# Kernel optimization log

Measured on AMD Instinct MI355X. Metric: run time of the kernel, lower is better.

Reference implementation:

```python
import jax, jax.numpy as jnp
import numpy as np

N = 100000   # vertices
T = 128      # temporal depth
E = 1600000  # edges (avg degree 16)
K = 9        # conv kernel size
PAD = 4      # 'same' padding -> T preserved
L = 3        # number of layers


def setup_inputs() -> dict:
    key = jax.random.key(0)
    ks = jax.random.split(key, 6)
    x = jax.random.normal(ks[0], (N, T), dtype=jnp.float32)
    edge_index = jax.random.randint(ks[1], (2, E), 0, N, dtype=jnp.int32)
    conv_w = jax.random.normal(ks[2], (L, 1, 1, K), dtype=jnp.float32) * (1.0 / np.sqrt(K))
    conv_b = jax.random.normal(ks[3], (L, 1), dtype=jnp.float32) * 0.1
    W_out = jax.random.normal(ks[4], (3, N), dtype=jnp.float32) * (1.0 / np.sqrt(N))
    b_out = jax.random.normal(ks[5], (3,), dtype=jnp.float32) * 0.1
    return {"x": x, "edge_index": edge_index, "conv_w": conv_w,
            "conv_b": conv_b, "W_out": W_out, "b_out": b_out}


def _conv1d(x, w, b):
    # x: [N, T], w: [1, 1, K] (OIH), b: [1]; torch Conv1d = cross-correlation.
    y = jax.lax.conv_general_dilated(
        x[:, None, :], w, window_strides=(1,), padding=[(PAD, PAD)],
        dimension_numbers=("NCH", "OIH", "NCH"))
    return y[:, 0, :] + b  # [N, T]


def reference(x, edge_index, conv_w, conv_b, W_out, b_out):
    # add_self_loops: append (i, i) for every node
    loop = jnp.arange(N, dtype=edge_index.dtype)
    src = jnp.concatenate([edge_index[0], loop])  # message sources
    dst = jnp.concatenate([edge_index[1], loop])  # aggregation targets
    # in-degree counts (>=1 due to self loops) for mean aggregation
    cnt = jax.ops.segment_sum(jnp.ones(src.shape, jnp.float32), dst,
                              num_segments=N)[:, None]  # [N, 1]
    for i in range(L):
        h = _conv1d(x, conv_w[i], conv_b[i])                    # [N, T]
        s = jax.ops.segment_sum(h[src], dst, num_segments=N)    # scatter-sum of gathered msgs
        x = jax.nn.relu(s / cnt)                                # mean aggr + relu
    x = x.reshape(-1, N)            # [T, N] (row-major view like torch .view)
    return x @ W_out.T + b_out      # [T, 3]
```

## Files before the change

### kernel.cpp

```cpp
#include <hip/hip_runtime.h>

#define NN 100000
#define TT 128
#define EE 1600000
#define KK 9
#define PADK 4
#define NSPLIT 16

#define BSH 7
#define BMASK 127
#define NBUCK 782
#define BCAP 2560
#define BINB 782
#define CVTB 12500

typedef _Float16 f16;
typedef __attribute__((ext_vector_type(2))) _Float16 f16x2;
typedef __attribute__((ext_vector_type(4))) _Float16 f16x4;
typedef __attribute__((ext_vector_type(8))) _Float16 f16x8;

union HU8 { f16x8 h; int4 i; };

__global__ void bin_cvt_kernel(const int* __restrict__ ei, int* __restrict__ gcursor,
                               unsigned int* __restrict__ binned,
                               const float4* __restrict__ x, f16x4* __restrict__ x16) {
    __shared__ int hist[NBUCK];
    __shared__ int gbase[NBUCK];
    int tid = threadIdx.x;

    if (blockIdx.x >= BINB) {
        int i = (blockIdx.x - BINB) * 256 + tid;
        float4 v = x[i];
        f16x4 o;
        o.x = (f16)v.x; o.y = (f16)v.y; o.z = (f16)v.z; o.w = (f16)v.w;
        x16[i] = o;
        return;
    }

    for (int i = tid; i < NBUCK; i += 256) hist[i] = 0;
    __syncthreads();
    int base = blockIdx.x * 2048;
    unsigned int val[8];
    int bkt[8];
    int rank[8];
#pragma unroll
    for (int k = 0; k < 8; k++) {
        int e = base + k * 256 + tid;
        bkt[k] = -1;
        if (e < EE) {
            int s = ei[e];
            int d = ei[EE + e];
            bkt[k] = d >> BSH;
            val[k] = ((unsigned int)(d & BMASK) << 20) | (unsigned int)s;
            rank[k] = atomicAdd(&hist[bkt[k]], 1);
        }
    }
    __syncthreads();
    for (int i = tid; i < NBUCK; i += 256)
        gbase[i] = hist[i] ? atomicAdd(&gcursor[i], hist[i]) : 0;
    __syncthreads();
#pragma unroll
    for (int k = 0; k < 8; k++) {
        if (bkt[k] >= 0)
            binned[(size_t)bkt[k] * BCAP + gbase[bkt[k]] + rank[k]] = val[k];
    }
}

__global__ void scanpart_kernel(const int* __restrict__ gcursor, int* __restrict__ part,
                                int* __restrict__ offsets) {
    __shared__ int sm[256];
    int tid = threadIdx.x;
    int base = tid * 4;
    int v[4];
    int s = 0;
#pragma unroll
    for (int k = 0; k < 4; k++) {
        int i = base + k;
        v[k] = (i < NBUCK) ? gcursor[i] : 0;
        s += v[k];
    }
    sm[tid] = s;
    __syncthreads();
    for (int off = 1; off < 256; off <<= 1) {
        int t = (tid >= off) ? sm[tid - off] : 0;
        __syncthreads();
        sm[tid] += t;
        __syncthreads();
    }
    int run = (tid == 0) ? 0 : sm[tid - 1];
#pragma unroll
    for (int k = 0; k < 4; k++) {
        int i = base + k;
        if (i < NBUCK) part[i] = run;
        run += v[k];
    }
    if (tid == 0) offsets[NN] = EE;
}

__global__ void bucket_csr_kernel(const unsigned int* __restrict__ binned,
                                  const int* __restrict__ gcursor,
                                  const int* __restrict__ part,
                                  int* __restrict__ offsets,
                                  float* __restrict__ inv_cnt,
                                  int* __restrict__ col) {
    __shared__ int hist[128];
    __shared__ int cur[128];
    __shared__ int sc[128];
    int b = blockIdx.x;
    int tid = threadIdx.x;
    int cnt = gcursor[b];
    const unsigned int* ePtr = binned + (size_t)b * BCAP;
    if (tid < 128) hist[tid] = 0;
    __syncthreads();
    for (int j = tid; j < cnt; j += 256)
        atomicAdd(&hist[ePtr[j] >> 20], 1);
    __syncthreads();
    int d = (tid < 128) ? hist[tid] : 0;
    if (tid < 128) sc[tid] = d;
    __syncthreads();
    for (int off = 1; off < 128; off <<= 1) {
        int t = (tid < 128 && tid >= off) ? sc[tid - off] : 0;
        __syncthreads();
        if (tid < 128) sc[tid] += t;
        __syncthreads();
    }
    if (tid < 128) {
        int node = (b << BSH) + tid;
        int pos = part[b] + sc[tid] - d;
        if (node < NN) {
            offsets[node] = pos;
            inv_cnt[node] = 1.0f / (1.0f + (float)d);
            cur[tid] = pos;
        }
    }
    __syncthreads();
    for (int j = tid; j < cnt; j += 256) {
        unsigned int v = ePtr[j];
        int pos = atomicAdd(&cur[v >> 20], 1);
        col[pos] = (int)(v & 0xFFFFF);
    }
}

__global__ void fused_layer_kernel(const f16x8* __restrict__ xin,
                                   const int* __restrict__ offsets,
                                   const int* __restrict__ col,
                                   const float* __restrict__ inv_cnt,
                                   const float* __restrict__ w9,
                                   const float* __restrict__ bptr,
                                   f16x8* __restrict__ yout) {
    int tid = threadIdx.x;
    int lane = tid & 63;
    int q = lane >> 4;
    int p = lane & 15;
    int node = blockIdx.x * 4 + (tid >> 6);

    int lo = offsets[node], hi = offsets[node + 1];
    int cnt = hi - lo;
    int my_col = (lane < cnt) ? col[lo + lane] : 0;
    int jn = cnt < 64 ? cnt : 64;

    const f16 z = (f16)0;
    f16x8 acc0 = {z, z, z, z, z, z, z, z};
    f16x8 acc1 = {z, z, z, z, z, z, z, z};

    int j = 0;
    for (; j + 7 < jn; j += 8) {
        int c0 = __shfl(my_col, j + q);
        int c1 = __shfl(my_col, j + 4 + q);
        f16x8 v0 = xin[(c0 << 4) | p];
        f16x8 v1 = xin[(c1 << 4) | p];
        acc0 += v0;
        acc1 += v1;
    }
    for (; j + 3 < jn; j += 4) {
        int c = __shfl(my_col, j + q);
        acc0 += xin[(c << 4) | p];
    }
    if (j < jn) {
        int rem = jn - j;
        int c = __shfl(my_col, j + (q < rem ? q : 0));
        f16x8 v = xin[(c << 4) | p];
        if (q < rem) acc1 += v;
    }
    for (int k = 64; k < cnt; k++) {
        int c = col[lo + k];
        f16x8 v = xin[(c << 4) | p];
        if (q == 0) acc0 += v;
    }
    acc0 += acc1;

    {
        HU8 u; u.h = acc0;
        int4 o;
        o.x = __shfl_xor(u.i.x, 16); o.y = __shfl_xor(u.i.y, 16);
        o.z = __shfl_xor(u.i.z, 16); o.w = __shfl_xor(u.i.w, 16);
        HU8 w; w.i = o;
        acc0 += w.h;
        u.h = acc0;
        o.x = __shfl_xor(u.i.x, 32); o.y = __shfl_xor(u.i.y, 32);
        o.z = __shfl_xor(u.i.z, 32); o.w = __shfl_xor(u.i.w, 32);
        w.i = o;
        acc0 += w.h;
    }

    f16x8 sv = xin[(node << 4) | p];
    float A[16];
    A[4]  = (float)acc0[0] + (float)sv[0];
    A[5]  = (float)acc0[1] + (float)sv[1];
    A[6]  = (float)acc0[2] + (float)sv[2];
    A[7]  = (float)acc0[3] + (float)sv[3];
    A[8]  = (float)acc0[4] + (float)sv[4];
    A[9]  = (float)acc0[5] + (float)sv[5];
    A[10] = (float)acc0[6] + (float)sv[6];
    A[11] = (float)acc0[7] + (float)sv[7];
#pragma unroll
    for (int i = 0; i < 4; i++) {
        A[i]      = __shfl_up(A[8 + i], 1, 16);
        A[12 + i] = __shfl_down(A[4 + i], 1, 16);
    }
    if (p == 0)  { A[0] = 0.0f; A[1] = 0.0f; A[2] = 0.0f; A[3] = 0.0f; }
    if (p == 15) { A[12] = 0.0f; A[13] = 0.0f; A[14] = 0.0f; A[15] = 0.0f; }

    float wr[KK];
#pragma unroll
    for (int k = 0; k < KK; k++) wr[k] = w9[k];
    float ic = inv_cnt[node];
    float b = bptr[0];
    f16x8 o;
#pragma unroll
    for (int i = 0; i < 8; i++) {
        float s = 0.0f;
#pragma unroll
        for (int k = 0; k < KK; k++) s += wr[k] * A[i + k];
        s = fmaxf(s * ic + b, 0.0f);
        o[i] = (f16)s;
    }
    if (q == 0) yout[(node << 4) | p] = o;
}

__global__ void out_kernel(const f16* __restrict__ y3, const float* __restrict__ Wout,
                           const float* __restrict__ bout, float* __restrict__ out) {
    int t = blockIdx.x;
    int sp = blockIdx.y;
    int tid = threadIdx.x;
    const int per = NN / NSPLIT;
    int lo = sp * per;
    int hi = lo + per;
    float a0 = 0.0f, a1 = 0.0f, a2 = 0.0f;
    for (int n = lo + tid * 2; n < hi; n += 512) {
        f16x2 v2 = *(const f16x2*)(y3 + (size_t)t * NN + n);
        float vx = (float)v2.x, vy = (float)v2.y;
        float2 wA = *(const float2*)(Wout + n);
        float2 wB = *(const float2*)(Wout + NN + n);
        float2 wC = *(const float2*)(Wout + 2 * NN + n);
        a0 += vx * wA.x + vy * wA.y;
        a1 += vx * wB.x + vy * wB.y;
        a2 += vx * wC.x + vy * wC.y;
    }
    for (int o = 32; o > 0; o >>= 1) {
        a0 += __shfl_down(a0, o);
        a1 += __shfl_down(a1, o);
        a2 += __shfl_down(a2, o);
    }
    __shared__ float red[4][3];
    int wave = tid >> 6;
    if ((tid & 63) == 0) {
        red[wave][0] = a0;
        red[wave][1] = a1;
        red[wave][2] = a2;
    }
    __syncthreads();
    if (tid == 0) {
        float r0 = red[0][0] + red[1][0] + red[2][0] + red[3][0];
        float r1 = red[0][1] + red[1][1] + red[2][1] + red[3][1];
        float r2 = red[0][2] + red[1][2] + red[2][2] + red[3][2];
        if (sp == 0) {
            r0 += bout[0];
            r1 += bout[1];
            r2 += bout[2];
        }
        atomicAdd(&out[t * 3 + 0], r0);
        atomicAdd(&out[t * 3 + 1], r1);
        atomicAdd(&out[t * 3 + 2], r2);
    }
}

extern "C" void kernel_launch(void* const* d_in, const int* in_sizes, int n_in,
                              void* d_out, int out_size, void* d_ws, size_t ws_size,
                              hipStream_t stream) {
    const float* x    = (const float*)d_in[0];
    const int*   ei   = (const int*)d_in[1];
    const float* cw   = (const float*)d_in[2];
    const float* cb   = (const float*)d_in[3];
    const float* Wout = (const float*)d_in[4];
    const float* bout = (const float*)d_in[5];
    float* out = (float*)d_out;

    char* ws = (char*)d_ws;
    size_t off = 0;
    auto alloc = [&](size_t bytes) -> void* {
        void* p = ws + off;
        off += (bytes + 255) & ~(size_t)255;
        return p;
    };
    f16*          x16     = (f16*)alloc((size_t)NN * TT * 2);
    f16*          yA      = (f16*)alloc((size_t)NN * TT * 2);
    f16*          yB      = (f16*)alloc((size_t)NN * TT * 2);
    unsigned int* binned  = (unsigned int*)alloc((size_t)NBUCK * BCAP * 4);
    int*          gcursor = (int*)alloc((size_t)NBUCK * 4);
    int*          part    = (int*)alloc((size_t)NBUCK * 4);
    int*          offsets = (int*)alloc((size_t)(NN + 1) * 4);
    float*        inv_cnt = (float*)alloc((size_t)NN * 4);
    int*          col     = (int*)alloc((size_t)EE * 4);

    hipMemsetAsync(gcursor, 0, (size_t)NBUCK * 4, stream);
    bin_cvt_kernel<<<BINB + CVTB, 256, 0, stream>>>(ei, gcursor, binned,
                                                    (const float4*)x, (f16x4*)x16);
    scanpart_kernel<<<1, 256, 0, stream>>>(gcursor, part, offsets);
    bucket_csr_kernel<<<NBUCK, 256, 0, stream>>>(binned, gcursor, part, offsets, inv_cnt, col);

    fused_layer_kernel<<<NN / 4, 256, 0, stream>>>((const f16x8*)x16, offsets, col, inv_cnt,
                                                   cw + 0 * KK, cb + 0, (f16x8*)yA);
    fused_layer_kernel<<<NN / 4, 256, 0, stream>>>((const f16x8*)yA, offsets, col, inv_cnt,
                                                   cw + 1 * KK, cb + 1, (f16x8*)yB);
    fused_layer_kernel<<<NN / 4, 256, 0, stream>>>((const f16x8*)yB, offsets, col, inv_cnt,
                                                   cw + 2 * KK, cb + 2, (f16x8*)yA);

    hipMemsetAsync(out, 0, (size_t)TT * 3 * 4, stream);
    out_kernel<<<dim3(TT, NSPLIT), 256, 0, stream>>>(yA, Wout, bout, out);
}
```

Before: 349.5 us.

## Fuse all stages into one persistent cooperative kernel with grid syncs

```diff
diff --git a/kernel.cpp b/kernel.cpp
--- a/kernel.cpp
+++ b/kernel.cpp
@@ -1,10 +1,12 @@
 #include <hip/hip_runtime.h>
+#include <hip/hip_cooperative_groups.h>
+
+namespace cg = cooperative_groups;
 
 #define NN 100000
 #define TT 128
 #define EE 1600000
 #define KK 9
-#define PADK 4
 #define NSPLIT 16
 
 #define BSH 7
@@ -21,279 +23,301 @@
 
 union HU8 { f16x8 h; int4 i; };
 
-__global__ void bin_cvt_kernel(const int* __restrict__ ei, int* __restrict__ gcursor,
-                               unsigned int* __restrict__ binned,
-                               const float4* __restrict__ x, f16x4* __restrict__ x16) {
-    __shared__ int hist[NBUCK];
-    __shared__ int gbase[NBUCK];
-    int tid = threadIdx.x;
-
-    if (blockIdx.x >= BINB) {
-        int i = (blockIdx.x - BINB) * 256 + tid;
-        float4 v = x[i];
-        f16x4 o;
-        o.x = (f16)v.x; o.y = (f16)v.y; o.z = (f16)v.z; o.w = (f16)v.w;
-        x16[i] = o;
-        return;
-    }
-
-    for (int i = tid; i < NBUCK; i += 256) hist[i] = 0;
-    __syncthreads();
-    int base = blockIdx.x * 2048;
-    unsigned int val[8];
-    int bkt[8];
-    int rank[8];
-#pragma unroll
-    for (int k = 0; k < 8; k++) {
-        int e = base + k * 256 + tid;
-        bkt[k] = -1;
-        if (e < EE) {
-            int s = ei[e];
-            int d = ei[EE + e];
-            bkt[k] = d >> BSH;
-            val[k] = ((unsigned int)(d & BMASK) << 20) | (unsigned int)s;
-            rank[k] = atomicAdd(&hist[bkt[k]], 1);
-        }
-    }
-    __syncthreads();
-    for (int i = tid; i < NBUCK; i += 256)
-        gbase[i] = hist[i] ? atomicAdd(&gcursor[i], hist[i]) : 0;
-    __syncthreads();
-#pragma unroll
-    for (int k = 0; k < 8; k++) {
-        if (bkt[k] >= 0)
-            binned[(size_t)bkt[k] * BCAP + gbase[bkt[k]] + rank[k]] = val[k];
-    }
-}
-
-__global__ void scanpart_kernel(const int* __restrict__ gcursor, int* __restrict__ part,
-                                int* __restrict__ offsets) {
-    __shared__ int sm[256];
-    int tid = threadIdx.x;
-    int base = tid * 4;
-    int v[4];
-    int s = 0;
-#pragma unroll
-    for (int k = 0; k < 4; k++) {
-        int i = base + k;
-        v[k] = (i < NBUCK) ? gcursor[i] : 0;
-        s += v[k];
-    }
-    sm[tid] = s;
-    __syncthreads();
-    for (int off = 1; off < 256; off <<= 1) {
-        int t = (tid >= off) ? sm[tid - off] : 0;
-        __syncthreads();
-        sm[tid] += t;
-        __syncthreads();
-    }
-    int run = (tid == 0) ? 0 : sm[tid - 1];
-#pragma unroll
-    for (int k = 0; k < 4; k++) {
-        int i = base + k;
-        if (i < NBUCK) part[i] = run;
-        run += v[k];
-    }
-    if (tid == 0) offsets[NN] = EE;
-}
-
-__global__ void bucket_csr_kernel(const unsigned int* __restrict__ binned,
-                                  const int* __restrict__ gcursor,
-                                  const int* __restrict__ part,
-                                  int* __restrict__ offsets,
-                                  float* __restrict__ inv_cnt,
-                                  int* __restrict__ col) {
-    __shared__ int hist[128];
-    __shared__ int cur[128];
-    __shared__ int sc[128];
-    int b = blockIdx.x;
-    int tid = threadIdx.x;
-    int cnt = gcursor[b];
-    const unsigned int* ePtr = binned + (size_t)b * BCAP;
-    if (tid < 128) hist[tid] = 0;
-    __syncthreads();
-    for (int j = tid; j < cnt; j += 256)
-        atomicAdd(&hist[ePtr[j] >> 20], 1);
-    __syncthreads();
-    int d = (tid < 128) ? hist[tid] : 0;
-    if (tid < 128) sc[tid] = d;
-    __syncthreads();
-    for (int off = 1; off < 128; off <<= 1) {
-        int t = (tid < 128 && tid >= off) ? sc[tid - off] : 0;
-        __syncthreads();
-        if (tid < 128) sc[tid] += t;
-        __syncthreads();
-    }
-    if (tid < 128) {
-        int node = (b << BSH) + tid;
-        int pos = part[b] + sc[tid] - d;
-        if (node < NN) {
-            offsets[node] = pos;
-            inv_cnt[node] = 1.0f / (1.0f + (float)d);
-            cur[tid] = pos;
-        }
-    }
-    __syncthreads();
-    for (int j = tid; j < cnt; j += 256) {
-        unsigned int v = ePtr[j];
-        int pos = atomicAdd(&cur[v >> 20], 1);
-        col[pos] = (int)(v & 0xFFFFF);
-    }
-}
-
-__global__ void fused_layer_kernel(const f16x8* __restrict__ xin,
-                                   const int* __restrict__ offsets,
-                                   const int* __restrict__ col,
-                                   const float* __restrict__ inv_cnt,
-                                   const float* __restrict__ w9,
-                                   const float* __restrict__ bptr,
-                                   f16x8* __restrict__ yout) {
+__device__ __forceinline__ void layer_stage(
+    const f16x8* __restrict__ xin,
+    const int* __restrict__ offsets, const int* __restrict__ col,
+    const float* __restrict__ inv_cnt,
+    const float* __restrict__ w9, const float* __restrict__ bptr,
+    f16x8* __restrict__ yout, int nwaves)
+{
     int tid = threadIdx.x;
     int lane = tid & 63;
     int q = lane >> 4;
     int p = lane & 15;
-    int node = blockIdx.x * 4 + (tid >> 6);
-
-    int lo = offsets[node], hi = offsets[node + 1];
-    int cnt = hi - lo;
-    int my_col = (lane < cnt) ? col[lo + lane] : 0;
-    int jn = cnt < 64 ? cnt : 64;
-
-    const f16 z = (f16)0;
-    f16x8 acc0 = {z, z, z, z, z, z, z, z};
-    f16x8 acc1 = {z, z, z, z, z, z, z, z};
-
-    int j = 0;
-    for (; j + 7 < jn; j += 8) {
-        int c0 = __shfl(my_col, j + q);
-        int c1 = __shfl(my_col, j + 4 + q);
-        f16x8 v0 = xin[(c0 << 4) | p];
-        f16x8 v1 = xin[(c1 << 4) | p];
-        acc0 += v0;
-        acc1 += v1;
-    }
-    for (; j + 3 < jn; j += 4) {
-        int c = __shfl(my_col, j + q);
-        acc0 += xin[(c << 4) | p];
-    }
-    if (j < jn) {
-        int rem = jn - j;
-        int c = __shfl(my_col, j + (q < rem ? q : 0));
-        f16x8 v = xin[(c << 4) | p];
-        if (q < rem) acc1 += v;
-    }
-    for (int k = 64; k < cnt; k++) {
-        int c = col[lo + k];
-        f16x8 v = xin[(c << 4) | p];
-        if (q == 0) acc0 += v;
-    }
-    acc0 += acc1;
-
-    {
-        HU8 u; u.h = acc0;
-        int4 o;
-        o.x = __shfl_xor(u.i.x, 16); o.y = __shfl_xor(u.i.y, 16);
-        o.z = __shfl_xor(u.i.z, 16); o.w = __shfl_xor(u.i.w, 16);
-        HU8 w; w.i = o;
-        acc0 += w.h;
-        u.h = acc0;
-        o.x = __shfl_xor(u.i.x, 32); o.y = __shfl_xor(u.i.y, 32);
-        o.z = __shfl_xor(u.i.z, 32); o.w = __shfl_xor(u.i.w, 32);
-        w.i = o;
-        acc0 += w.h;
-    }
-
-    f16x8 sv = xin[(node << 4) | p];
-    float A[16];
-    A[4]  = (float)acc0[0] + (float)sv[0];
-    A[5]  = (float)acc0[1] + (float)sv[1];
-    A[6]  = (float)acc0[2] + (float)sv[2];
-    A[7]  = (float)acc0[3] + (float)sv[3];
-    A[8]  = (float)acc0[4] + (float)sv[4];
-    A[9]  = (float)acc0[5] + (float)sv[5];
-    A[10] = (float)acc0[6] + (float)sv[6];
-    A[11] = (float)acc0[7] + (float)sv[7];
-#pragma unroll
-    for (int i = 0; i < 4; i++) {
-        A[i]      = __shfl_up(A[8 + i], 1, 16);
-        A[12 + i] = __shfl_down(A[4 + i], 1, 16);
-    }
-    if (p == 0)  { A[0] = 0.0f; A[1] = 0.0f; A[2] = 0.0f; A[3] = 0.0f; }
-    if (p == 15) { A[12] = 0.0f; A[13] = 0.0f; A[14] = 0.0f; A[15] = 0.0f; }
-
     float wr[KK];
 #pragma unroll
     for (int k = 0; k < KK; k++) wr[k] = w9[k];
-    float ic = inv_cnt[node];
-    float b = bptr[0];
-    f16x8 o;
-#pragma unroll
-    for (int i = 0; i < 8; i++) {
-        float s = 0.0f;
-#pragma unroll
-        for (int k = 0; k < KK; k++) s += wr[k] * A[i + k];
-        s = fmaxf(s * ic + b, 0.0f);
-        o[i] = (f16)s;
-    }
-    if (q == 0) yout[(node << 4) | p] = o;
+    float bb = bptr[0];
+
+    for (int node = (blockIdx.x << 2) | (tid >> 6); node < NN; node += nwaves) {
+        int lo = offsets[node], hi = offsets[node + 1];
+        int cnt = hi - lo;
+        int my_col = (lane < cnt) ? col[lo + lane] : 0;
+        int jn = cnt < 64 ? cnt : 64;
+
+        const f16 z = (f16)0;
+        f16x8 acc0 = {z, z, z, z, z, z, z, z};
+        f16x8 acc1 = {z, z, z, z, z, z, z, z};
+
+        int j = 0;
+        for (; j + 7 < jn; j += 8) {
+            int c0 = __shfl(my_col, j + q);
+            int c1 = __shfl(my_col, j + 4 + q);
+            f16x8 v0 = xin[(c0 << 4) | p];
+            f16x8 v1 = xin[(c1 << 4) | p];
+            acc0 += v0;
+            acc1 += v1;
+        }
+        for (; j + 3 < jn; j += 4) {
+            int c = __shfl(my_col, j + q);
+            acc0 += xin[(c << 4) | p];
+        }
+        if (j < jn) {
+            int rem = jn - j;
+            int c = __shfl(my_col, j + (q < rem ? q : 0));
+            f16x8 v = xin[(c << 4) | p];
+            if (q < rem) acc1 += v;
+        }
+        for (int k = 64; k < cnt; k++) {
+            int c = col[lo + k];
+            f16x8 v = xin[(c << 4) | p];
+            if (q == 0) acc0 += v;
+        }
+        acc0 += acc1;
+
+        {
+            HU8 u; u.h = acc0;
+            int4 o;
+            o.x = __shfl_xor(u.i.x, 16); o.y = __shfl_xor(u.i.y, 16);
+            o.z = __shfl_xor(u.i.z, 16); o.w = __shfl_xor(u.i.w, 16);
+            HU8 w2; w2.i = o;
+            acc0 += w2.h;
+            u.h = acc0;
+            o.x = __shfl_xor(u.i.x, 32); o.y = __shfl_xor(u.i.y, 32);
+            o.z = __shfl_xor(u.i.z, 32); o.w = __shfl_xor(u.i.w, 32);
+            w2.i = o;
+            acc0 += w2.h;
+        }
+
+        f16x8 sv = xin[(node << 4) | p];
+        float A[16];
+        A[4]  = (float)acc0[0] + (float)sv[0];
+        A[5]  = (float)acc0[1] + (float)sv[1];
+        A[6]  = (float)acc0[2] + (float)sv[2];
+        A[7]  = (float)acc0[3] + (float)sv[3];
+        A[8]  = (float)acc0[4] + (float)sv[4];
+        A[9]  = (float)acc0[5] + (float)sv[5];
+        A[10] = (float)acc0[6] + (float)sv[6];
+        A[11] = (float)acc0[7] + (float)sv[7];
+#pragma unroll
+        for (int i = 0; i < 4; i++) {
+            A[i]      = __shfl_up(A[8 + i], 1, 16);
+            A[12 + i] = __shfl_down(A[4 + i], 1, 16);
+        }
+        if (p == 0)  { A[0] = 0.0f; A[1] = 0.0f; A[2] = 0.0f; A[3] = 0.0f; }
+        if (p == 15) { A[12] = 0.0f; A[13] = 0.0f; A[14] = 0.0f; A[15] = 0.0f; }
+
+        float ic = inv_cnt[node];
+        f16x8 o8;
+#pragma unroll
+        for (int i = 0; i < 8; i++) {
+            float s = 0.0f;
+#pragma unroll
+            for (int k = 0; k < KK; k++) s += wr[k] * A[i + k];
+            s = fmaxf(s * ic + bb, 0.0f);
+            o8[i] = (f16)s;
+        }
+        if (q == 0) yout[(node << 4) | p] = o8;
+    }
 }
 
-__global__ void out_kernel(const f16* __restrict__ y3, const float* __restrict__ Wout,
-                           const float* __restrict__ bout, float* __restrict__ out) {
-    int t = blockIdx.x;
-    int sp = blockIdx.y;
+__global__ __launch_bounds__(256, 8)
+void mega_kernel(const int* __restrict__ ei, const float4* __restrict__ x,
+                 const float* __restrict__ cw, const float* __restrict__ cb,
+                 const float* __restrict__ Wout, const float* __restrict__ bout,
+                 float* __restrict__ out,
+                 f16x8* __restrict__ x16, f16x8* __restrict__ yA, f16x8* __restrict__ yB,
+                 unsigned int* __restrict__ binned, int* __restrict__ gcursor,
+                 int* __restrict__ part, int* __restrict__ offsets,
+                 float* __restrict__ inv_cnt, int* __restrict__ col)
+{
+    cg::grid_group grid = cg::this_grid();
+    __shared__ int binh[NBUCK];
+    __shared__ int gbase[NBUCK];
+    __shared__ int sm[256];
+    __shared__ int bukh[128];
+    __shared__ int cur[128];
+    __shared__ int sc[128];
+    __shared__ float red[4][3];
+
     int tid = threadIdx.x;
-    const int per = NN / NSPLIT;
-    int lo = sp * per;
-    int hi = lo + per;
-    float a0 = 0.0f, a1 = 0.0f, a2 = 0.0f;
-    for (int n = lo + tid * 2; n < hi; n += 512) {
-        f16x2 v2 = *(const f16x2*)(y3 + (size_t)t * NN + n);
-        float vx = (float)v2.x, vy = (float)v2.y;
-        float2 wA = *(const float2*)(Wout + n);
-        float2 wB = *(const float2*)(Wout + NN + n);
-        float2 wC = *(const float2*)(Wout + 2 * NN + n);
-        a0 += vx * wA.x + vy * wA.y;
-        a1 += vx * wB.x + vy * wB.y;
-        a2 += vx * wC.x + vy * wC.y;
-    }
-    for (int o = 32; o > 0; o >>= 1) {
-        a0 += __shfl_down(a0, o);
-        a1 += __shfl_down(a1, o);
-        a2 += __shfl_down(a2, o);
-    }
-    __shared__ float red[4][3];
-    int wave = tid >> 6;
-    if ((tid & 63) == 0) {
-        red[wave][0] = a0;
-        red[wave][1] = a1;
-        red[wave][2] = a2;
-    }
-    __syncthreads();
-    if (tid == 0) {
-        float r0 = red[0][0] + red[1][0] + red[2][0] + red[3][0];
-        float r1 = red[0][1] + red[1][1] + red[2][1] + red[3][1];
-        float r2 = red[0][2] + red[1][2] + red[2][2] + red[3][2];
-        if (sp == 0) {
-            r0 += bout[0];
-            r1 += bout[1];
-            r2 += bout[2];
-        }
-        atomicAdd(&out[t * 3 + 0], r0);
-        atomicAdd(&out[t * 3 + 1], r1);
-        atomicAdd(&out[t * 3 + 2], r2);
+    int blk = blockIdx.x;
+    int nblk = gridDim.x;
+    int gid = blk * 256 + tid;
+
+    for (int i = gid; i < NBUCK; i += nblk * 256) gcursor[i] = 0;
+    for (int i = gid; i < TT * 3; i += nblk * 256) out[i] = 0.0f;
+    grid.sync();
+
+    for (int vb = blk; vb < BINB + CVTB; vb += nblk) {
+        if (vb < BINB) {
+            for (int i = tid; i < NBUCK; i += 256) binh[i] = 0;
+            __syncthreads();
+            int base = vb * 2048;
+            unsigned int val[8];
+            int bkt[8];
+            int rank[8];
+#pragma unroll
+            for (int k = 0; k < 8; k++) {
+                int e = base + k * 256 + tid;
+                bkt[k] = -1;
+                if (e < EE) {
+                    int s = ei[e];
+                    int d = ei[EE + e];
+                    bkt[k] = d >> BSH;
+                    val[k] = ((unsigned int)(d & BMASK) << 20) | (unsigned int)s;
+                    rank[k] = atomicAdd(&binh[bkt[k]], 1);
+                }
+            }
+            __syncthreads();
+            for (int i = tid; i < NBUCK; i += 256)
+                gbase[i] = binh[i] ? atomicAdd(&gcursor[i], binh[i]) : 0;
+            __syncthreads();
+#pragma unroll
+            for (int k = 0; k < 8; k++) {
+                if (bkt[k] >= 0)
+                    binned[(size_t)bkt[k] * BCAP + gbase[bkt[k]] + rank[k]] = val[k];
+            }
+            __syncthreads();
+        } else {
+            int i = (vb - BINB) * 256 + tid;
+            float4 v = x[i];
+            f16x4 o;
+            o.x = (f16)v.x; o.y = (f16)v.y; o.z = (f16)v.z; o.w = (f16)v.w;
+            ((f16x4*)x16)[i] = o;
+        }
+    }
+    grid.sync();
+
+    if (blk == 0) {
+        int base = tid * 4;
+        int v[4];
+        int s = 0;
+#pragma unroll
+        for (int k = 0; k < 4; k++) {
+            int i = base + k;
+            v[k] = (i < NBUCK) ? gcursor[i] : 0;
+            s += v[k];
+        }
+        sm[tid] = s;
+        __syncthreads();
+        for (int off = 1; off < 256; off <<= 1) {
+            int t = (tid >= off) ? sm[tid - off] : 0;
+            __syncthreads();
+            sm[tid] += t;
+            __syncthreads();
+        }
+        int run = (tid == 0) ? 0 : sm[tid - 1];
+#pragma unroll
+        for (int k = 0; k < 4; k++) {
+            int i = base + k;
+            if (i < NBUCK) part[i] = run;
+            run += v[k];
+        }
+        if (tid == 0) offsets[NN] = EE;
+    }
+    grid.sync();
+
+    for (int b = blk; b < NBUCK; b += nblk) {
+        int cnt = gcursor[b];
+        const unsigned int* ePtr = binned + (size_t)b * BCAP;
+        if (tid < 128) bukh[tid] = 0;
+        __syncthreads();
+        for (int j = tid; j < cnt; j += 256)
+            atomicAdd(&bukh[ePtr[j] >> 20], 1);
+        __syncthreads();
+        int d = (tid < 128) ? bukh[tid] : 0;
+        if (tid < 128) sc[tid] = d;
+        __syncthreads();
+        for (int off = 1; off < 128; off <<= 1) {
+            int t = (tid < 128 && tid >= off) ? sc[tid - off] : 0;
+            __syncthreads();
+            if (tid < 128) sc[tid] += t;
+            __syncthreads();
+        }
+        if (tid < 128) {
+            int node = (b << BSH) + tid;
+            int pos = part[b] + sc[tid] - d;
+            if (node < NN) {
+                offsets[node] = pos;
+                inv_cnt[node] = 1.0f / (1.0f + (float)d);
+                cur[tid] = pos;
+            }
+        }
+        __syncthreads();
+        for (int j = tid; j < cnt; j += 256) {
+            unsigned int v = ePtr[j];
+            int pos = atomicAdd(&cur[v >> 20], 1);
+            col[pos] = (int)(v & 0xFFFFF);
+        }
+        __syncthreads();
+    }
+    grid.sync();
+
+    int nwaves = nblk * 4;
+    layer_stage(x16, offsets, col, inv_cnt, cw + 0 * KK, cb + 0, yA, nwaves);
+    grid.sync();
+    layer_stage(yA, offsets, col, inv_cnt, cw + 1 * KK, cb + 1, yB, nwaves);
+    grid.sync();
+    layer_stage(yB, offsets, col, inv_cnt, cw + 2 * KK, cb + 2, yA, nwaves);
+    grid.sync();
+
+    const f16* y3 = (const f16*)yA;
+    for (int vb = blk; vb < TT * NSPLIT; vb += nblk) {
+        int t = vb >> 4;
+        int sp = vb & 15;
+        const int per = NN / NSPLIT;
+        int lo = sp * per;
+        int hi = lo + per;
+        float a0 = 0.0f, a1 = 0.0f, a2 = 0.0f;
+        for (int n = lo + tid * 2; n < hi; n += 512) {
+            f16x2 v2 = *(const f16x2*)(y3 + (size_t)t * NN + n);
+            float vx = (float)v2.x, vy = (float)v2.y;
+            float2 wA = *(const float2*)(Wout + n);
+            float2 wB = *(const float2*)(Wout + NN + n);
+            float2 wC = *(const float2*)(Wout + 2 * NN + n);
+            a0 += vx * wA.x + vy * wA.y;
+            a1 += vx * wB.x + vy * wB.y;
+            a2 += vx * wC.x + vy * wC.y;
+        }
+        for (int o = 32; o > 0; o >>= 1) {
+            a0 += __shfl_down(a0, o);
+            a1 += __shfl_down(a1, o);
+            a2 += __shfl_down(a2, o);
+        }
+        int wave = tid >> 6;
+        if ((tid & 63) == 0) {
+            red[wave][0] = a0;
+            red[wave][1] = a1;
+            red[wave][2] = a2;
+        }
+        __syncthreads();
+        if (tid == 0) {
+            float r0 = red[0][0] + red[1][0] + red[2][0] + red[3][0];
+            float r1 = red[0][1] + red[1][1] + red[2][1] + red[3][1];
+            float r2 = red[0][2] + red[1][2] + red[2][2] + red[3][2];
+            if (sp == 0) {
+                r0 += bout[0];
+                r1 += bout[1];
+                r2 += bout[2];
+            }
+            atomicAdd(&out[t * 3 + 0], r0);
+            atomicAdd(&out[t * 3 + 1], r1);
+            atomicAdd(&out[t * 3 + 2], r2);
+        }
+        __syncthreads();
     }
 }
 
 extern "C" void kernel_launch(void* const* d_in, const int* in_sizes, int n_in,
                               void* d_out, int out_size, void* d_ws, size_t ws_size,
                               hipStream_t stream) {
-    const float* x    = (const float*)d_in[0];
-    const int*   ei   = (const int*)d_in[1];
-    const float* cw   = (const float*)d_in[2];
-    const float* cb   = (const float*)d_in[3];
-    const float* Wout = (const float*)d_in[4];
-    const float* bout = (const float*)d_in[5];
+    const int*    ei   = (const int*)d_in[1];
+    const float4* x    = (const float4*)d_in[0];
+    const float*  cw   = (const float*)d_in[2];
+    const float*  cb   = (const float*)d_in[3];
+    const float*  Wout = (const float*)d_in[4];
+    const float*  bout = (const float*)d_in[5];
     float* out = (float*)d_out;
 
     char* ws = (char*)d_ws;
@@ -303,9 +327,9 @@
         off += (bytes + 255) & ~(size_t)255;
         return p;
     };
-    f16*          x16     = (f16*)alloc((size_t)NN * TT * 2);
-    f16*          yA      = (f16*)alloc((size_t)NN * TT * 2);
-    f16*          yB      = (f16*)alloc((size_t)NN * TT * 2);
+    f16x8*        x16     = (f16x8*)alloc((size_t)NN * TT * 2);
+    f16x8*        yA      = (f16x8*)alloc((size_t)NN * TT * 2);
+    f16x8*        yB      = (f16x8*)alloc((size_t)NN * TT * 2);
     unsigned int* binned  = (unsigned int*)alloc((size_t)NBUCK * BCAP * 4);
     int*          gcursor = (int*)alloc((size_t)NBUCK * 4);
     int*          part    = (int*)alloc((size_t)NBUCK * 4);
@@ -313,19 +337,20 @@
     float*        inv_cnt = (float*)alloc((size_t)NN * 4);
     int*          col     = (int*)alloc((size_t)EE * 4);
 
-    hipMemsetAsync(gcursor, 0, (size_t)NBUCK * 4, stream);
-    bin_cvt_kernel<<<BINB + CVTB, 256, 0, stream>>>(ei, gcursor, binned,
-                                                    (const float4*)x, (f16x4*)x16);
-    scanpart_kernel<<<1, 256, 0, stream>>>(gcursor, part, offsets);
-    bucket_csr_kernel<<<NBUCK, 256, 0, stream>>>(binned, gcursor, part, offsets, inv_cnt, col);
-
-    fused_layer_kernel<<<NN / 4, 256, 0, stream>>>((const f16x8*)x16, offsets, col, inv_cnt,
-                                                   cw + 0 * KK, cb + 0, (f16x8*)yA);
-    fused_layer_kernel<<<NN / 4, 256, 0, stream>>>((const f16x8*)yA, offsets, col, inv_cnt,
-                                                   cw + 1 * KK, cb + 1, (f16x8*)yB);
-    fused_layer_kernel<<<NN / 4, 256, 0, stream>>>((const f16x8*)yB, offsets, col, inv_cnt,
-                                                   cw + 2 * KK, cb + 2, (f16x8*)yA);
-
-    hipMemsetAsync(out, 0, (size_t)TT * 3 * 4, stream);
-    out_kernel<<<dim3(TT, NSPLIT), 256, 0, stream>>>(yA, Wout, bout, out);
+    int nb = 0;
+    int cgrid = 2048;
+    if (hipOccupancyMaxActiveBlocksPerMultiprocessor(&nb, mega_kernel, 256, 0) == hipSuccess
+        && nb > 0) {
+        int m = nb * 256;
+        if (m < cgrid) cgrid = m;
+    }
+
+    void* args[] = {
+        (void*)&ei, (void*)&x, (void*)&cw, (void*)&cb, (void*)&Wout, (void*)&bout,
+        (void*)&out, (void*)&x16, (void*)&yA, (void*)&yB,
+        (void*)&binned, (void*)&gcursor, (void*)&part, (void*)&offsets,
+        (void*)&inv_cnt, (void*)&col
+    };
+    hipLaunchCooperativeKernel((void*)mega_kernel, dim3(cgrid), dim3(256),
+                               args, 0, stream);
 }
```

Measured after the change: 1.218 ms. 3.48x slower.
